# Kernel optimization log

Measured on AMD Instinct MI355X. Metric: run time of the kernel, lower is better.

The kernel has to match this reference:

```python
import jax, jax.numpy as jnp
import numpy as np

N = 50000       # nodes
E = 800000      # edges (avg degree 16)
R = 8           # relations
IN = 128        # in_channels
H = 128         # hidden_size
B = 10          # graphs in batch
NPG = N // B    # nodes per graph (equal-size graphs)
NEG_SLOPE = 0.2 # RGATConv default negative_slope


def setup_inputs() -> dict:
    key = jax.random.key(0)
    ks = jax.random.split(key, 12)
    s = 0.1
    x = jax.random.normal(ks[0], (N, IN), dtype=jnp.float32)
    edge_index = jax.random.randint(ks[1], (2, E), 0, N, dtype=jnp.int32)
    edge_type = jax.random.randint(ks[2], (E,), 0, R, dtype=jnp.int32)
    batch = jnp.repeat(jnp.arange(B, dtype=jnp.int32), NPG)
    W1 = jax.random.normal(ks[3], (R, IN, H), dtype=jnp.float32) * s
    q1 = jax.random.normal(ks[4], (H, 1), dtype=jnp.float32) * s
    k1 = jax.random.normal(ks[5], (H, 1), dtype=jnp.float32) * s
    b1 = jnp.zeros((H,), dtype=jnp.float32)
    W2 = jax.random.normal(ks[6], (R, H, H), dtype=jnp.float32) * s
    q2 = jax.random.normal(ks[7], (H, 1), dtype=jnp.float32) * s
    k2 = jax.random.normal(ks[8], (H, 1), dtype=jnp.float32) * s
    b2 = jnp.zeros((H,), dtype=jnp.float32)
    Wl = jax.random.normal(ks[9], (H, H), dtype=jnp.float32) * s
    bl = jnp.zeros((H,), dtype=jnp.float32)
    return dict(x=x, edge_index=edge_index, edge_type=edge_type, batch=batch,
                W1=W1, q1=q1, k1=k1, b1=b1, W2=W2, q2=q2, k2=k2, b2=b2,
                Wl=Wl, bl=bl)


def _rgat_conv(x, src, tgt, etype, W, q, k, b):
    # Per-relation transform once per node ([R,N,H]), then gather per edge;
    # mathematically identical to PyG's per-edge bmm but avoids the [E,in,H] blowup.
    xW = jnp.einsum('ni,rio->rno', x, W)          # [R, N, H]
    outi = xW[etype, tgt]                          # [E, H] transformed target feats
    outj = xW[etype, src]                          # [E, H] transformed source feats
    # additive self-attention, heads=1, dim=1
    alpha = jax.nn.leaky_relu(outi @ q + outj @ k, NEG_SLOPE)  # [E, 1]
    # across-relation segment softmax over incoming edges of each target node
    m = jax.ops.segment_max(alpha, tgt, num_segments=N)        # [N, 1]
    a = jnp.exp(alpha - m[tgt])
    den = jax.ops.segment_sum(a, tgt, num_segments=N)          # [N, 1]
    a = a / (den[tgt] + 1e-16)
    out = jax.ops.segment_sum(a * outj, tgt, num_segments=N)   # [N, H]
    return out + b


def reference(x, edge_index, edge_type, batch, W1, q1, k1, b1,
              W2, q2, k2, b2, Wl, bl):
    src, tgt = edge_index[0], edge_index[1]
    h = jax.nn.relu(_rgat_conv(x, src, tgt, edge_type, W1, q1, k1, b1))
    # dropout p=0 -> identity
    h = jax.nn.relu(_rgat_conv(h, src, tgt, edge_type, W2, q2, k2, b2))
    h = h @ Wl.T + bl                               # nn.Linear
    # to_dense_batch: batch is sorted with equal-size graphs of NPG nodes
    return h.reshape(B, NPG, H)
```

## Files before the change

### kernel.cpp

```cpp
#include <hip/hip_runtime.h>


typedef unsigned int uint;
typedef unsigned short ushort_t;

using bf16x8 = __attribute__((ext_vector_type(8))) __bf16;
using f32x4  = __attribute__((ext_vector_type(4))) float;

__device__ __forceinline__ ushort_t fToBf(float f) {
  uint u = __float_as_uint(f);
  u += 0x7FFFu + ((u >> 16) & 1);
  return (ushort_t)(u >> 16);
}
__device__ __forceinline__ float bfToF(ushort_t h) {
  return __uint_as_float(((uint)h) << 16);
}


__global__ void k_count(const int* __restrict__ tgt, int* __restrict__ deg, int E) {
  int e = blockIdx.x * 256 + threadIdx.x;
  if (e < E) atomicAdd(&deg[tgt[e]], 1);
}

__global__ void k_scanA(const int* __restrict__ deg, int* __restrict__ incl,
                        int* __restrict__ bsum, int n) {
  __shared__ int s[256];
  int tid = threadIdx.x;
  int i = blockIdx.x * 256 + tid;
  int v = (i < n) ? deg[i] : 0;
  s[tid] = v;
  __syncthreads();
  for (int off = 1; off < 256; off <<= 1) {
    int t = (tid >= off) ? s[tid - off] : 0;
    __syncthreads();
    s[tid] += t;
    __syncthreads();
  }
  if (i < n) incl[i] = s[tid];
  if (tid == 255) bsum[blockIdx.x] = s[255];
}

__global__ void k_scanB(int* __restrict__ bsum, int nb) {
  __shared__ int s[256];
  int tid = threadIdx.x;
  int v = (tid < nb) ? bsum[tid] : 0;
  s[tid] = v;
  __syncthreads();
  for (int off = 1; off < 256; off <<= 1) {
    int t = (tid >= off) ? s[tid - off] : 0;
    __syncthreads();
    s[tid] += t;
    __syncthreads();
  }
  if (tid < nb) bsum[tid] = s[tid] - v;
}

__global__ void k_scanC(const int* __restrict__ deg, const int* __restrict__ incl,
                        const int* __restrict__ bsum, int* __restrict__ rowptr,
                        int n, int E) {
  int i = blockIdx.x * 256 + threadIdx.x;
  if (i < n) {
    rowptr[i] = bsum[blockIdx.x] + incl[i] - deg[i];
    if (i == n - 1) rowptr[n] = E;
  }
}

__global__ void k_scatter(const int* __restrict__ src, const int* __restrict__ tgt,
                          const int* __restrict__ et, const int* __restrict__ rowptr,
                          int* __restrict__ cursor, int* __restrict__ sorted, int E) {
  int e = blockIdx.x * 256 + threadIdx.x;
  if (e >= E) return;
  int t = tgt[e];
  int pos = atomicAdd(&cursor[t], 1);
  sorted[rowptr[t] + pos] = src[e] | (et[e] << 16);
}


__global__ void k_cvt(const float* __restrict__ in, ushort_t* __restrict__ out, int n4) {
  int i = blockIdx.x * 256 + threadIdx.x;
  if (i >= n4) return;
  float4 v = ((const float4*)in)[i];
  ushort4 o;
  o.x = fToBf(v.x); o.y = fToBf(v.y); o.z = fToBf(v.z); o.w = fToBf(v.w);
  ((ushort4*)out)[i] = o;
}

__global__ void k_wT(const float* __restrict__ W, ushort_t* __restrict__ WT) {
  int rn = blockIdx.x;
  int r = rn >> 7, n = rn & 127;
  int k = threadIdx.x;
  WT[(size_t)rn * 128 + k] = fToBf(W[((size_t)r * 128 + k) * 128 + n]);
}

__global__ void k_wqwk(const float* __restrict__ W, const float* __restrict__ q,
                       const float* __restrict__ k, ushort_t* __restrict__ wqk) {
  int g = blockIdx.x * 256 + threadIdx.x;
  if (g >= 2048) return;
  int which = g >> 10;
  int idx = g & 1023;
  const float* w = W + (size_t)idx * 128;
  const float* v = which ? k : q;
  float s = 0.f;
  #pragma unroll 8
  for (int h = 0; h < 128; h++) s += w[h] * v[h];
  int r = idx >> 7, kin = idx & 127;
  wqk[((which << 3) + r) * 128 + kin] = fToBf(s);
}


#define LDA 136

__global__ __launch_bounds__(256) void
k_gemm8(const ushort_t* __restrict__ A, const ushort_t* __restrict__ BT8,
        const ushort_t* __restrict__ Wqk, ushort_t* __restrict__ xW,
        float* __restrict__ stbl, int M) {
  __shared__ ushort_t As[64 * LDA];
  __shared__ ushort_t Bs[128 * LDA];
  int tid = threadIdx.x;
  int row0 = blockIdx.x * 64;

  for (int c = tid; c < 1024; c += 256) {
    int r = c >> 4, off = (c & 15) * 8;
    int4 v = {0, 0, 0, 0};
    if (row0 + r < M) v = *(const int4*)(A + (size_t)(row0 + r) * 128 + off);
    *(int4*)(As + r * LDA + off) = v;
  }
  for (int c = tid; c < 2048; c += 256) {
    int nn = c >> 4, off = (c & 15) * 8;
    *(int4*)(Bs + nn * LDA + off) = *(const int4*)(BT8 + (size_t)nn * 128 + off);
  }
  __syncthreads();

  int wv = tid >> 6, lane = tid & 63;
  int l15 = lane & 15, quad = lane >> 4;
  int wr = wv * 16;

  bf16x8 afr[4];
  #pragma unroll
  for (int kb = 0; kb < 4; kb++)
    afr[kb] = *reinterpret_cast<const bf16x8*>(As + (wr + l15) * LDA + kb * 32 + quad * 8);

  for (int r = 0; r < 8; r++) {
    f32x4 acc[8] = {};
    #pragma unroll
    for (int ct = 0; ct < 8; ct++) {
      #pragma unroll
      for (int kb = 0; kb < 4; kb++) {
        bf16x8 bfr = *reinterpret_cast<const bf16x8*>(Bs + (ct * 16 + l15) * LDA + kb * 32 + quad * 8);
        acc[ct] = __builtin_amdgcn_mfma_f32_16x16x32_bf16(afr[kb], bfr, acc[ct], 0, 0, 0);
      }
    }
    __syncthreads();
    #pragma unroll
    for (int ct = 0; ct < 8; ct++)
      #pragma unroll
      for (int reg = 0; reg < 4; reg++)
        As[(wr + quad * 4 + reg) * LDA + ct * 16 + l15] = fToBf(acc[ct][reg]);
    const ushort_t* nb = (r < 7) ? (BT8 + (size_t)(r + 1) * 16384) : Wqk;
    int lim = (r < 7) ? 2048 : 256;
    for (int c = tid; c < lim; c += 256) {
      int nn = c >> 4, off = (c & 15) * 8;
      *(int4*)(Bs + nn * LDA + off) = *(const int4*)(nb + (size_t)nn * 128 + off);
    }
    __syncthreads();
    for (int c = tid; c < 1024; c += 256) {
      int rr = c >> 4, off = (c & 15) * 8;
      if (row0 + rr < M)
        *(int4*)(xW + ((size_t)r * M + row0 + rr) * 128 + off) = *(const int4*)(As + rr * LDA + off);
    }
  }

  f32x4 acc = {};
  #pragma unroll
  for (int kb = 0; kb < 4; kb++) {
    bf16x8 bfr = *reinterpret_cast<const bf16x8*>(Bs + l15 * LDA + kb * 32 + quad * 8);
    acc = __builtin_amdgcn_mfma_f32_16x16x32_bf16(afr[kb], bfr, acc, 0, 0, 0);
  }
  #pragma unroll
  for (int reg = 0; reg < 4; reg++) {
    int rr = row0 + wr + quad * 4 + reg;
    if (rr < M) stbl[(size_t)rr * 16 + l15] = acc[reg];
  }
}

__global__ __launch_bounds__(256) void
k_gemmL(const ushort_t* __restrict__ A, const ushort_t* __restrict__ BT,
        float* __restrict__ Cout, const float* __restrict__ bias, int M) {
  __shared__ ushort_t As[64 * LDA];
  __shared__ ushort_t Bs[128 * LDA];
  int tid = threadIdx.x;
  int row0 = blockIdx.x * 64;
  for (int c = tid; c < 1024; c += 256) {
    int r = c >> 4, off = (c & 15) * 8;
    int4 v = {0, 0, 0, 0};
    if (row0 + r < M) v = *(const int4*)(A + (size_t)(row0 + r) * 128 + off);
    *(int4*)(As + r * LDA + off) = v;
  }
  for (int c = tid; c < 2048; c += 256) {
    int nn = c >> 4, off = (c & 15) * 8;
    *(int4*)(Bs + nn * LDA + off) = *(const int4*)(BT + (size_t)nn * 128 + off);
  }
  __syncthreads();
  int wv = tid >> 6, lane = tid & 63;
  int l15 = lane & 15, quad = lane >> 4;
  int wr = wv * 16;
  bf16x8 afr[4];
  #pragma unroll
  for (int kb = 0; kb < 4; kb++)
    afr[kb] = *reinterpret_cast<const bf16x8*>(As + (wr + l15) * LDA + kb * 32 + quad * 8);
  f32x4 acc[8] = {};
  #pragma unroll
  for (int ct = 0; ct < 8; ct++)
    #pragma unroll
    for (int kb = 0; kb < 4; kb++) {
      bf16x8 bfr = *reinterpret_cast<const bf16x8*>(Bs + (ct * 16 + l15) * LDA + kb * 32 + quad * 8);
      acc[ct] = __builtin_amdgcn_mfma_f32_16x16x32_bf16(afr[kb], bfr, acc[ct], 0, 0, 0);
    }
  #pragma unroll
  for (int ct = 0; ct < 8; ct++)
    #pragma unroll
    for (int reg = 0; reg < 4; reg++) {
      int rr = row0 + wr + quad * 4 + reg;
      if (rr < M) ((float*)Cout)[(size_t)rr * 128 + ct * 16 + l15] = acc[ct][reg] + bias[ct * 16 + l15];
    }
}


#define ACC8(W_, V_)                                                     \
  acc[0] += W_ * bfToF((ushort_t)(V_.x & 0xFFFF));                       \
  acc[1] += W_ * bfToF((ushort_t)(V_.x >> 16));                          \
  acc[2] += W_ * bfToF((ushort_t)(V_.y & 0xFFFF));                       \
  acc[3] += W_ * bfToF((ushort_t)(V_.y >> 16));                          \
  acc[4] += W_ * bfToF((ushort_t)(V_.z & 0xFFFF));                       \
  acc[5] += W_ * bfToF((ushort_t)(V_.z >> 16));                          \
  acc[6] += W_ * bfToF((ushort_t)(V_.w & 0xFFFF));                       \
  acc[7] += W_ * bfToF((ushort_t)(V_.w >> 16));

__global__ __launch_bounds__(256) void
k_aggr(const ushort_t* __restrict__ feat,
       const float* __restrict__ stbl,
       const int* __restrict__ rowptr, const int* __restrict__ sorted,
       const float* __restrict__ bias, ushort_t* __restrict__ outp, int n) {
  int tid = threadIdx.x, wv = tid >> 6, lane = tid & 63;
  int t = blockIdx.x * 4 + wv;
  if (t >= n) return;
  int e0 = rowptr[t], e1 = rowptr[t + 1];
  int g4 = lane >> 4, fcol = lane & 15;

  float m = -INFINITY, den = 0.f;
  float acc[8] = {};

  for (int base = e0; base < e1; base += 64) {
    int cnt = min(64, e1 - base);
    float alpha = -INFINITY;
    int pk = 0;
    if (lane < cnt) {
      pk = sorted[base + lane];
      int s = pk & 0xFFFF, r = pk >> 16;
      float a = stbl[(size_t)t * 16 + r] + stbl[(size_t)s * 16 + 8 + r];
      alpha = (a >= 0.f) ? a : 0.2f * a;
    }
    float cm = alpha;
    #pragma unroll
    for (int off = 32; off; off >>= 1) cm = fmaxf(cm, __shfl_xor(cm, off, 64));
    float nm = fmaxf(m, cm);
    float sc = __expf(m - nm);
    den *= sc;
    #pragma unroll
    for (int i = 0; i < 8; i++) acc[i] *= sc;
    float w = (lane < cnt) ? __expf(alpha - nm) : 0.f;
    float ws = w;
    #pragma unroll
    for (int off = 32; off; off >>= 1) ws += __shfl_xor(ws, off, 64);
    den += ws;
    m = nm;

    for (int g = 0; g < cnt; g += 16) {
      int i0 = g + g4;
      float w0 = __shfl(w, i0, 64);
      float w1 = __shfl(w, i0 + 4, 64);
      float w2 = __shfl(w, i0 + 8, 64);
      float w3 = __shfl(w, i0 + 12, 64);
      int p0 = __shfl(pk, i0, 64);
      int p1 = __shfl(pk, i0 + 4, 64);
      int p2 = __shfl(pk, i0 + 8, 64);
      int p3 = __shfl(pk, i0 + 12, 64);
      const uint4* r0 = (const uint4*)(feat + (size_t)((p0 >> 16) * n + (p0 & 0xFFFF)) * 128) + fcol;
      const uint4* r1 = (const uint4*)(feat + (size_t)((p1 >> 16) * n + (p1 & 0xFFFF)) * 128) + fcol;
      const uint4* r2 = (const uint4*)(feat + (size_t)((p2 >> 16) * n + (p2 & 0xFFFF)) * 128) + fcol;
      const uint4* r3 = (const uint4*)(feat + (size_t)((p3 >> 16) * n + (p3 & 0xFFFF)) * 128) + fcol;
      uint4 v0 = *r0;
      uint4 v1 = *r1;
      uint4 v2 = *r2;
      uint4 v3 = *r3;
      ACC8(w0, v0)
      ACC8(w1, v1)
      ACC8(w2, v2)
      ACC8(w3, v3)
    }
  }

  #pragma unroll
  for (int i = 0; i < 8; i++) acc[i] += __shfl_xor(acc[i], 16, 64);
  #pragma unroll
  for (int i = 0; i < 8; i++) acc[i] += __shfl_xor(acc[i], 32, 64);

  float inv = (den > 0.f) ? 1.f / (den + 1e-16f) : 0.f;
  uint4 o;
  uint* op = (uint*)&o;
  #pragma unroll
  for (int j = 0; j < 4; j++) {
    float a0 = fmaxf(acc[2 * j] * inv + bias[fcol * 8 + 2 * j], 0.f);
    float a1 = fmaxf(acc[2 * j + 1] * inv + bias[fcol * 8 + 2 * j + 1], 0.f);
    op[j] = (uint)fToBf(a0) | ((uint)fToBf(a1) << 16);
  }
  if (lane < 16) *(uint4*)(outp + (size_t)t * 128 + fcol * 8) = o;
}


extern "C" void kernel_launch(void* const* d_in, const int* in_sizes, int n_in,
                              void* d_out, int out_size, void* d_ws, size_t ws_size,
                              hipStream_t stream) {
  const float* x   = (const float*)d_in[0];
  const int* ei    = (const int*)d_in[1];
  const int* etype = (const int*)d_in[2];
  const float* W1  = (const float*)d_in[4];
  const float* q1  = (const float*)d_in[5];
  const float* k1  = (const float*)d_in[6];
  const float* b1  = (const float*)d_in[7];
  const float* W2  = (const float*)d_in[8];
  const float* q2  = (const float*)d_in[9];
  const float* k2  = (const float*)d_in[10];
  const float* b2  = (const float*)d_in[11];
  const float* Wl  = (const float*)d_in[12];
  const float* bl  = (const float*)d_in[13];
  float* out       = (float*)d_out;

  const int N = in_sizes[0] / 128;
  const int E = in_sizes[2];

  char* ws = (char*)d_ws;
  size_t off = 0;
  auto alloc = [&](size_t bytes) {
    size_t o = off;
    off = (off + bytes + 255) & ~(size_t)255;
    return o;
  };

  ushort_t* xbf   = (ushort_t*)(ws + alloc((size_t)N * 128 * 2));
  ushort_t* xW    = (ushort_t*)(ws + alloc((size_t)8 * N * 128 * 2));
  ushort_t* h1    = (ushort_t*)(ws + alloc((size_t)N * 128 * 2));
  ushort_t* h2    = (ushort_t*)(ws + alloc((size_t)N * 128 * 2));
  ushort_t* w1t   = (ushort_t*)(ws + alloc(8 * 128 * 128 * 2));
  ushort_t* w2t   = (ushort_t*)(ws + alloc(8 * 128 * 128 * 2));
  ushort_t* wlt   = (ushort_t*)(ws + alloc(128 * 128 * 2));
  ushort_t* wqk1  = (ushort_t*)(ws + alloc(16 * 128 * 2));
  ushort_t* wqk2  = (ushort_t*)(ws + alloc(16 * 128 * 2));
  float* stbl     = (float*)(ws + alloc((size_t)N * 16 * 4));
  int* deg        = (int*)(ws + alloc((size_t)N * 4));
  int* cursor     = (int*)(ws + alloc((size_t)N * 4));
  int* incl       = (int*)(ws + alloc((size_t)N * 4));
  int* rowptr     = (int*)(ws + alloc((size_t)(N + 1) * 4));
  int* bsum       = (int*)(ws + alloc(256 * 4));
  int* sorted     = (int*)(ws + alloc((size_t)E * 4));
  (void)ws_size; (void)n_in; (void)out_size;

  const int* srcp = ei;
  const int* tgtp = ei + E;

  int gE = (E + 255) / 256;
  int gN = (N + 255) / 256;
  int gW = (N + 3) / 4;
  int gM = (N + 63) / 64;

  hipMemsetAsync(deg, 0, (size_t)N * 4, stream);
  hipMemsetAsync(cursor, 0, (size_t)N * 4, stream);
  k_count<<<gE, 256, 0, stream>>>(tgtp, deg, E);
  k_scanA<<<gN, 256, 0, stream>>>(deg, incl, bsum, N);
  k_scanB<<<1, 256, 0, stream>>>(bsum, gN);
  k_scanC<<<gN, 256, 0, stream>>>(deg, incl, bsum, rowptr, N, E);
  k_scatter<<<gE, 256, 0, stream>>>(srcp, tgtp, etype, rowptr, cursor, sorted, E);

  k_cvt<<<(N * 128 / 4 + 255) / 256, 256, 0, stream>>>(x, xbf, N * 128 / 4);
  k_wT<<<1024, 128, 0, stream>>>(W1, w1t);
  k_wT<<<1024, 128, 0, stream>>>(W2, w2t);
  k_cvt<<<(128 * 128 / 4 + 255) / 256, 256, 0, stream>>>(Wl, wlt, 128 * 128 / 4);
  k_wqwk<<<8, 256, 0, stream>>>(W1, q1, k1, wqk1);
  k_wqwk<<<8, 256, 0, stream>>>(W2, q2, k2, wqk2);

  k_gemm8<<<gM, 256, 0, stream>>>(xbf, w1t, wqk1, xW, stbl, N);
  k_aggr<<<gW, 256, 0, stream>>>(xW, stbl, rowptr, sorted, b1, h1, N);

  k_gemm8<<<gM, 256, 0, stream>>>(h1, w2t, wqk2, xW, stbl, N);
  k_aggr<<<gW, 256, 0, stream>>>(xW, stbl, rowptr, sorted, b2, h2, N);

  k_gemmL<<<gM, 256, 0, stream>>>(h2, wlt, out, bl, N);
}
```

Measured before the change: 445.4 us.

## Restructure relation GEMM to register-resident node tiles and fuse conversions

The relation-transform GEMM is rewritten so each wave holds 32 node rows of input in registers and streams weight fragments directly from global memory (L2), with no block-wide shared staging or syncthreads. Shared memory is used only as a per-wave buffer to repack outputs into coalesced stores. The fp32-to-bf16 conversion of x is fused into the first GEMM, Wl conversion is fused into the final linear kernel, and the per-layer weight prep launches are merged, cutting kernel launches and an intermediate buffer. The cost is repeated global/L2 reads of the weight tiles by every wave, and reliance on occupancy hints.

```diff
diff --git a/kernel.cpp b/kernel.cpp
--- a/kernel.cpp
+++ b/kernel.cpp
@@ -76,115 +76,126 @@
 }
 
 
-__global__ void k_cvt(const float* __restrict__ in, ushort_t* __restrict__ out, int n4) {
-  int i = blockIdx.x * 256 + threadIdx.x;
-  if (i >= n4) return;
-  float4 v = ((const float4*)in)[i];
-  ushort4 o;
-  o.x = fToBf(v.x); o.y = fToBf(v.y); o.z = fToBf(v.z); o.w = fToBf(v.w);
-  ((ushort4*)out)[i] = o;
-}
-
-__global__ void k_wT(const float* __restrict__ W, ushort_t* __restrict__ WT) {
-  int rn = blockIdx.x;
+__global__ void k_wT(const float* __restrict__ W1, const float* __restrict__ W2,
+                     ushort_t* __restrict__ WT) {
+  int b = blockIdx.x;
+  const float* W = (b >= 1024) ? W2 : W1;
+  int rn = b & 1023;
   int r = rn >> 7, n = rn & 127;
   int k = threadIdx.x;
-  WT[(size_t)rn * 128 + k] = fToBf(W[((size_t)r * 128 + k) * 128 + n]);
-}
-
-__global__ void k_wqwk(const float* __restrict__ W, const float* __restrict__ q,
-                       const float* __restrict__ k, ushort_t* __restrict__ wqk) {
+  WT[(size_t)b * 128 + k] = fToBf(W[((size_t)r * 128 + k) * 128 + n]);
+}
+
+__global__ void k_wqwk(const float* __restrict__ W1, const float* __restrict__ q1,
+                       const float* __restrict__ k1, const float* __restrict__ W2,
+                       const float* __restrict__ q2, const float* __restrict__ k2,
+                       ushort_t* __restrict__ wqk) {
   int g = blockIdx.x * 256 + threadIdx.x;
-  if (g >= 2048) return;
-  int which = g >> 10;
+  if (g >= 4096) return;
+  int layer = g >> 11;
+  int which = (g >> 10) & 1;
   int idx = g & 1023;
-  const float* w = W + (size_t)idx * 128;
-  const float* v = which ? k : q;
+  const float* w = (layer ? W2 : W1) + (size_t)idx * 128;
+  const float* v = layer ? (which ? k2 : q2) : (which ? k1 : q1);
   float s = 0.f;
   #pragma unroll 8
   for (int h = 0; h < 128; h++) s += w[h] * v[h];
   int r = idx >> 7, kin = idx & 127;
-  wqk[((which << 3) + r) * 128 + kin] = fToBf(s);
+  wqk[(size_t)layer * 2048 + ((which << 3) + r) * 128 + kin] = fToBf(s);
 }
 
 
 #define LDA 136
 
-__global__ __launch_bounds__(256) void
-k_gemm8(const ushort_t* __restrict__ A, const ushort_t* __restrict__ BT8,
+template <bool F32IN>
+__global__ __launch_bounds__(256, 3) void
+k_gemm8(const void* __restrict__ Ain, const ushort_t* __restrict__ WT,
         const ushort_t* __restrict__ Wqk, ushort_t* __restrict__ xW,
         float* __restrict__ stbl, int M) {
-  __shared__ ushort_t As[64 * LDA];
-  __shared__ ushort_t Bs[128 * LDA];
-  int tid = threadIdx.x;
-  int row0 = blockIdx.x * 64;
-
-  for (int c = tid; c < 1024; c += 256) {
-    int r = c >> 4, off = (c & 15) * 8;
-    int4 v = {0, 0, 0, 0};
-    if (row0 + r < M) v = *(const int4*)(A + (size_t)(row0 + r) * 128 + off);
-    *(int4*)(As + r * LDA + off) = v;
-  }
-  for (int c = tid; c < 2048; c += 256) {
-    int nn = c >> 4, off = (c & 15) * 8;
-    *(int4*)(Bs + nn * LDA + off) = *(const int4*)(BT8 + (size_t)nn * 128 + off);
-  }
-  __syncthreads();
-
-  int wv = tid >> 6, lane = tid & 63;
+  __shared__ ushort_t rp[4][32 * LDA];
+  int tid = threadIdx.x, wv = tid >> 6, lane = tid & 63;
   int l15 = lane & 15, quad = lane >> 4;
-  int wr = wv * 16;
-
-  bf16x8 afr[4];
-  #pragma unroll
-  for (int kb = 0; kb < 4; kb++)
-    afr[kb] = *reinterpret_cast<const bf16x8*>(As + (wr + l15) * LDA + kb * 32 + quad * 8);
-
-  for (int r = 0; r < 8; r++) {
-    f32x4 acc[8] = {};
-    #pragma unroll
-    for (int ct = 0; ct < 8; ct++) {
+  int node0 = blockIdx.x * 128 + wv * 32;
+  ushort_t* rpw = rp[wv];
+
+  bf16x8 bx[2][4];
+  #pragma unroll
+  for (int nt = 0; nt < 2; nt++) {
+    int node = node0 + nt * 16 + l15;
+    if (node >= M) node = M - 1;
+    if (F32IN) {
+      const float* row = (const float*)Ain + (size_t)node * 128;
       #pragma unroll
       for (int kb = 0; kb < 4; kb++) {
-        bf16x8 bfr = *reinterpret_cast<const bf16x8*>(Bs + (ct * 16 + l15) * LDA + kb * 32 + quad * 8);
-        acc[ct] = __builtin_amdgcn_mfma_f32_16x16x32_bf16(afr[kb], bfr, acc[ct], 0, 0, 0);
+        float4 a = *(const float4*)(row + kb * 32 + quad * 8);
+        float4 b = *(const float4*)(row + kb * 32 + quad * 8 + 4);
+        union { bf16x8 v; ushort_t u[8]; } t;
+        t.u[0] = fToBf(a.x); t.u[1] = fToBf(a.y); t.u[2] = fToBf(a.z); t.u[3] = fToBf(a.w);
+        t.u[4] = fToBf(b.x); t.u[5] = fToBf(b.y); t.u[6] = fToBf(b.z); t.u[7] = fToBf(b.w);
+        bx[nt][kb] = t.v;
       }
-    }
-    __syncthreads();
-    #pragma unroll
-    for (int ct = 0; ct < 8; ct++)
+    } else {
+      const ushort_t* row = (const ushort_t*)Ain + (size_t)node * 128;
       #pragma unroll
-      for (int reg = 0; reg < 4; reg++)
-        As[(wr + quad * 4 + reg) * LDA + ct * 16 + l15] = fToBf(acc[ct][reg]);
-    const ushort_t* nb = (r < 7) ? (BT8 + (size_t)(r + 1) * 16384) : Wqk;
-    int lim = (r < 7) ? 2048 : 256;
-    for (int c = tid; c < lim; c += 256) {
-      int nn = c >> 4, off = (c & 15) * 8;
-      *(int4*)(Bs + nn * LDA + off) = *(const int4*)(nb + (size_t)nn * 128 + off);
-    }
-    __syncthreads();
-    for (int c = tid; c < 1024; c += 256) {
-      int rr = c >> 4, off = (c & 15) * 8;
-      if (row0 + rr < M)
-        *(int4*)(xW + ((size_t)r * M + row0 + rr) * 128 + off) = *(const int4*)(As + rr * LDA + off);
-    }
-  }
-
-  f32x4 acc = {};
-  #pragma unroll
-  for (int kb = 0; kb < 4; kb++) {
-    bf16x8 bfr = *reinterpret_cast<const bf16x8*>(Bs + l15 * LDA + kb * 32 + quad * 8);
-    acc = __builtin_amdgcn_mfma_f32_16x16x32_bf16(afr[kb], bfr, acc, 0, 0, 0);
-  }
-  #pragma unroll
-  for (int reg = 0; reg < 4; reg++) {
-    int rr = row0 + wr + quad * 4 + reg;
-    if (rr < M) stbl[(size_t)rr * 16 + l15] = acc[reg];
+      for (int kb = 0; kb < 4; kb++)
+        bx[nt][kb] = *(const bf16x8*)(row + kb * 32 + quad * 8);
+    }
+  }
+
+  for (int r = 0; r < 8; r++) {
+    const ushort_t* Wr = WT + (size_t)r * 16384;
+    f32x4 acc0[8] = {}, acc1[8] = {};
+    #pragma unroll
+    for (int mt = 0; mt < 8; mt++) {
+      bf16x8 af[4];
+      #pragma unroll
+      for (int kb = 0; kb < 4; kb++)
+        af[kb] = *(const bf16x8*)(Wr + (size_t)(mt * 16 + l15) * 128 + kb * 32 + quad * 8);
+      #pragma unroll
+      for (int kb = 0; kb < 4; kb++) {
+        acc0[mt] = __builtin_amdgcn_mfma_f32_16x16x32_bf16(af[kb], bx[0][kb], acc0[mt], 0, 0, 0);
+        acc1[mt] = __builtin_amdgcn_mfma_f32_16x16x32_bf16(af[kb], bx[1][kb], acc1[mt], 0, 0, 0);
+      }
+    }
+    #pragma unroll
+    for (int mt = 0; mt < 8; mt++) {
+      uint2 p0, p1;
+      p0.x = (uint)fToBf(acc0[mt][0]) | ((uint)fToBf(acc0[mt][1]) << 16);
+      p0.y = (uint)fToBf(acc0[mt][2]) | ((uint)fToBf(acc0[mt][3]) << 16);
+      p1.x = (uint)fToBf(acc1[mt][0]) | ((uint)fToBf(acc1[mt][1]) << 16);
+      p1.y = (uint)fToBf(acc1[mt][2]) | ((uint)fToBf(acc1[mt][3]) << 16);
+      *(uint2*)(rpw + (size_t)l15 * LDA + mt * 16 + quad * 4) = p0;
+      *(uint2*)(rpw + (size_t)(16 + l15) * LDA + mt * 16 + quad * 4) = p1;
+    }
+    #pragma unroll
+    for (int i = 0; i < 8; i++) {
+      int row = i * 4 + quad;
+      int off = l15 * 8;
+      int node = node0 + row;
+      if (node < M) {
+        int4 v = *(const int4*)(rpw + (size_t)row * LDA + off);
+        *(int4*)(xW + ((size_t)r * M + node) * 128 + off) = v;
+      }
+    }
+  }
+
+  bf16x8 aq[4];
+  #pragma unroll
+  for (int kb = 0; kb < 4; kb++)
+    aq[kb] = *(const bf16x8*)(Wqk + (size_t)l15 * 128 + kb * 32 + quad * 8);
+  #pragma unroll
+  for (int nt = 0; nt < 2; nt++) {
+    f32x4 acc = {};
+    #pragma unroll
+    for (int kb = 0; kb < 4; kb++)
+      acc = __builtin_amdgcn_mfma_f32_16x16x32_bf16(aq[kb], bx[nt][kb], acc, 0, 0, 0);
+    int node = node0 + nt * 16 + l15;
+    if (node < M) *(float4*)(stbl + (size_t)node * 16 + quad * 4) = *(float4*)&acc;
   }
 }
 
 __global__ __launch_bounds__(256) void
-k_gemmL(const ushort_t* __restrict__ A, const ushort_t* __restrict__ BT,
+k_gemmL(const ushort_t* __restrict__ A, const float* __restrict__ Wl,
         float* __restrict__ Cout, const float* __restrict__ bias, int M) {
   __shared__ ushort_t As[64 * LDA];
   __shared__ ushort_t Bs[128 * LDA];
@@ -198,7 +209,11 @@
   }
   for (int c = tid; c < 2048; c += 256) {
     int nn = c >> 4, off = (c & 15) * 8;
-    *(int4*)(Bs + nn * LDA + off) = *(const int4*)(BT + (size_t)nn * 128 + off);
+    float4 a = *(const float4*)(Wl + (size_t)nn * 128 + off);
+    float4 b = *(const float4*)(Wl + (size_t)nn * 128 + off + 4);
+    ushort_t* d = Bs + nn * LDA + off;
+    d[0] = fToBf(a.x); d[1] = fToBf(a.y); d[2] = fToBf(a.z); d[3] = fToBf(a.w);
+    d[4] = fToBf(b.x); d[5] = fToBf(b.y); d[6] = fToBf(b.z); d[7] = fToBf(b.w);
   }
   __syncthreads();
   int wv = tid >> 6, lane = tid & 63;
@@ -221,7 +236,7 @@
     #pragma unroll
     for (int reg = 0; reg < 4; reg++) {
       int rr = row0 + wr + quad * 4 + reg;
-      if (rr < M) ((float*)Cout)[(size_t)rr * 128 + ct * 16 + l15] = acc[ct][reg] + bias[ct * 16 + l15];
+      if (rr < M) Cout[(size_t)rr * 128 + ct * 16 + l15] = acc[ct][reg] + bias[ct * 16 + l15];
     }
 }
 
@@ -347,15 +362,11 @@
     return o;
   };
 
-  ushort_t* xbf   = (ushort_t*)(ws + alloc((size_t)N * 128 * 2));
   ushort_t* xW    = (ushort_t*)(ws + alloc((size_t)8 * N * 128 * 2));
   ushort_t* h1    = (ushort_t*)(ws + alloc((size_t)N * 128 * 2));
   ushort_t* h2    = (ushort_t*)(ws + alloc((size_t)N * 128 * 2));
-  ushort_t* w1t   = (ushort_t*)(ws + alloc(8 * 128 * 128 * 2));
-  ushort_t* w2t   = (ushort_t*)(ws + alloc(8 * 128 * 128 * 2));
-  ushort_t* wlt   = (ushort_t*)(ws + alloc(128 * 128 * 2));
-  ushort_t* wqk1  = (ushort_t*)(ws + alloc(16 * 128 * 2));
-  ushort_t* wqk2  = (ushort_t*)(ws + alloc(16 * 128 * 2));
+  ushort_t* wT    = (ushort_t*)(ws + alloc((size_t)2 * 8 * 128 * 128 * 2));
+  ushort_t* wqk   = (ushort_t*)(ws + alloc(2 * 16 * 128 * 2));
   float* stbl     = (float*)(ws + alloc((size_t)N * 16 * 4));
   int* deg        = (int*)(ws + alloc((size_t)N * 4));
   int* cursor     = (int*)(ws + alloc((size_t)N * 4));
@@ -368,10 +379,11 @@
   const int* srcp = ei;
   const int* tgtp = ei + E;
 
-  int gE = (E + 255) / 256;
-  int gN = (N + 255) / 256;
-  int gW = (N + 3) / 4;
-  int gM = (N + 63) / 64;
+  int gE  = (E + 255) / 256;
+  int gN  = (N + 255) / 256;
+  int gW  = (N + 3) / 4;
+  int gM  = (N + 63) / 64;
+  int gM2 = (N + 127) / 128;
 
   hipMemsetAsync(deg, 0, (size_t)N * 4, stream);
   hipMemsetAsync(cursor, 0, (size_t)N * 4, stream);
@@ -381,18 +393,15 @@
   k_scanC<<<gN, 256, 0, stream>>>(deg, incl, bsum, rowptr, N, E);
   k_scatter<<<gE, 256, 0, stream>>>(srcp, tgtp, etype, rowptr, cursor, sorted, E);
 
-  k_cvt<<<(N * 128 / 4 + 255) / 256, 256, 0, stream>>>(x, xbf, N * 128 / 4);
-  k_wT<<<1024, 128, 0, stream>>>(W1, w1t);
-  k_wT<<<1024, 128, 0, stream>>>(W2, w2t);
-  k_cvt<<<(128 * 128 / 4 + 255) / 256, 256, 0, stream>>>(Wl, wlt, 128 * 128 / 4);
-  k_wqwk<<<8, 256, 0, stream>>>(W1, q1, k1, wqk1);
-  k_wqwk<<<8, 256, 0, stream>>>(W2, q2, k2, wqk2);
-
-  k_gemm8<<<gM, 256, 0, stream>>>(xbf, w1t, wqk1, xW, stbl, N);
+  k_wT<<<2048, 128, 0, stream>>>(W1, W2, wT);
+  k_wqwk<<<16, 256, 0, stream>>>(W1, q1, k1, W2, q2, k2, wqk);
+
+  k_gemm8<true><<<gM2, 256, 0, stream>>>(x, wT, wqk, xW, stbl, N);
   k_aggr<<<gW, 256, 0, stream>>>(xW, stbl, rowptr, sorted, b1, h1, N);
 
-  k_gemm8<<<gM, 256, 0, stream>>>(h1, w2t, wqk2, xW, stbl, N);
+  k_gemm8<false><<<gM2, 256, 0, stream>>>(h1, wT + (size_t)8 * 128 * 128,
+                                          wqk + 2048, xW, stbl, N);
   k_aggr<<<gW, 256, 0, stream>>>(xW, stbl, rowptr, sorted, b2, h2, N);
 
-  k_gemmL<<<gM, 256, 0, stream>>>(h2, wlt, out, bl, N);
-}
+  k_gemmL<<<gM, 256, 0, stream>>>(h2, Wl, out, bl, N);
+}
```

Result: no change. 439.6 us (-1.3%).
